# Kernel optimization log

Hardware: AMD Instinct MI355X
Metric: run time of the kernel (lower is better)

Reference implementation:

```python
import math
import jax, jax.numpy as jnp
import numpy as np


def _pairwise_sqdist(x, y):
    # x: [N, d], y: [M, d] -> [N, M]
    x2 = jnp.sum(x * x, axis=-1)[:, None]
    y2 = jnp.sum(y * y, axis=-1)[None, :]
    return jnp.maximum(x2 + y2 - 2.0 * (x @ y.T), 0.0)


def setup_inputs() -> dict:
    key = jax.random.key(0)
    k1, k2 = jax.random.split(key)
    N, M, D = 8192, 8192, 2
    base_points = jax.random.normal(k1, (N, D), dtype=jnp.float32)
    target_points = jax.random.normal(k2, (M, D), dtype=jnp.float32)
    log_sigma = jnp.asarray(math.log(0.1), dtype=jnp.float32)
    log_scale = jnp.zeros((D,), dtype=jnp.float32)
    return {
        "base_points": base_points,
        "target_points": target_points,
        "log_sigma": log_sigma,
        "log_scale": log_scale,
    }


def reference(base_points, target_points, log_sigma, log_scale):
    # learn_scale=True: anisotropic per-coordinate scaling
    scale = jnp.exp(log_scale)
    base = base_points * scale
    target = target_points * scale

    # uniform node weights (use_weight_net=False)
    N = base.shape[0]
    M = target.shape[0]
    w_base = jnp.full((N,), 1.0 / N, dtype=base.dtype)
    w_target = jnp.full((M,), 1.0 / M, dtype=target.dtype)

    # center=True: subtract weighted centroid of each cloud
    base = base - jnp.sum(w_base[:, None] * base, axis=0, keepdims=True)
    target = target - jnp.sum(w_target[:, None] * target, axis=0, keepdims=True)

    sigma = jnp.exp(log_sigma)
    inv2s2 = 1.0 / (2.0 * sigma * sigma)

    k_bb = jnp.exp(-_pairwise_sqdist(base, base) * inv2s2)      # [N, N]
    k_tt = jnp.exp(-_pairwise_sqdist(target, target) * inv2s2)  # [M, M]
    k_bt = jnp.exp(-_pairwise_sqdist(base, target) * inv2s2)    # [N, M]

    term_bb = w_base @ (k_bb @ w_base)
    term_tt = w_target @ (k_tt @ w_target)
    term_bt = w_base @ (k_bt @ w_target)
    loss = term_bb + term_tt - 2.0 * term_bt
    return loss
```

## Files before the change

### kernel.cpp

```cpp
#include <hip/hip_runtime.h>


#define BLOCK 256
#define NT_CROSS 512
#define NT_TOT   1056
#define LOG2E 1.4426950408889634f

typedef float v2f __attribute__((ext_vector_type(2)));

struct Prep { float f0, f1, sh0, sh1; };

__device__ __forceinline__ float fexp2(float x) {
    return __builtin_amdgcn_exp2f(x);
}

__global__ __launch_bounds__(1024) void prep_kernel(
    const float* __restrict__ base, const float* __restrict__ target,
    const float* __restrict__ log_sigma, const float* __restrict__ log_scale,
    int N, int M, Prep* __restrict__ pp, double* __restrict__ slots)
{
    __shared__ double mred[16][4];
    const int tid = threadIdx.x;
    if (tid < 64) slots[tid] = 0.0;

    double sbx = 0, sby = 0, stx = 0, sty = 0;
    const float4* b4 = (const float4*)base;
    const float4* t4 = (const float4*)target;
    for (int i = tid; i < (N >> 1); i += 1024) {
        float4 v = b4[i];
        sbx += (double)v.x + (double)v.z;
        sby += (double)v.y + (double)v.w;
    }
    for (int i = tid; i < (M >> 1); i += 1024) {
        float4 v = t4[i];
        stx += (double)v.x + (double)v.z;
        sty += (double)v.y + (double)v.w;
    }
    for (int off = 32; off; off >>= 1) {
        sbx += __shfl_down(sbx, off); sby += __shfl_down(sby, off);
        stx += __shfl_down(stx, off); sty += __shfl_down(sty, off);
    }
    if ((tid & 63) == 0) {
        mred[tid >> 6][0] = sbx; mred[tid >> 6][1] = sby;
        mred[tid >> 6][2] = stx; mred[tid >> 6][3] = sty;
    }
    __syncthreads();
    if (tid == 0) {
        double b0 = 0, b1 = 0, t0 = 0, t1 = 0;
        for (int k = 0; k < 16; ++k) {
            b0 += mred[k][0]; b1 += mred[k][1];
            t0 += mred[k][2]; t1 += mred[k][3];
        }
        float s0 = expf(log_scale[0]);
        float s1 = expf(log_scale[1]);
        float sigma = expf(log_sigma[0]);
        float inv2s2 = 1.0f / (2.0f * sigma * sigma);
        float sq = sqrtf(inv2s2 * LOG2E);
        float f0 = s0 * sq, f1 = s1 * sq;
        pp->f0 = f0; pp->f1 = f1;
        pp->sh0 = (float)(b0 / (double)N - t0 / (double)M) * f0;
        pp->sh1 = (float)(b1 / (double)N - t1 / (double)M) * f1;
    }
}

__global__ __launch_bounds__(BLOCK, 4) void mmd_main(
    const float* __restrict__ base, const float* __restrict__ target,
    int N, int M, const Prep* __restrict__ pp, double* __restrict__ slots)
{
    __shared__ __align__(16) float tbx[256];
    __shared__ __align__(16) float tby[256];
    __shared__ __align__(16) float tbc[256];
    __shared__ double wredd[4];

    const int tid = threadIdx.x;
    const int t   = blockIdx.x;
    const Prep p = *pp;
    const float2* base2   = (const float2*)base;
    const float2* target2 = (const float2*)target;

    const double wNN = 1.0 / ((double)N * (double)N);
    const double wMM = 1.0 / ((double)M * (double)M);
    const double wNM = -2.0 / ((double)N * (double)M);

    int ib, jb, term;
    bool diag;
    const float2* A2;
    const float2* B2;
    double wt;
    float shx = 0.f, shy = 0.f;
    if (t < NT_CROSS) {
        ib = t >> 5; jb = t & 31;
        A2 = base2; B2 = target2;
        wt = wNM; diag = false; term = 2;
        shx = p.sh0; shy = p.sh1;
    } else {
        const int u = t - NT_CROSS;
        term = (u >= 272) ? 1 : 0;
        const int v = u - term * 272;
        int r = (int)((33.0f - sqrtf(1089.0f - 4.0f * (float)v)) * 0.5f);
        r = min(max(r, 0), 15);
        while (r > 0 && r * (33 - r) > v) --r;
        while (r < 15 && (r + 1) * (32 - r) <= v) ++r;
        ib = r;
        jb = 2 * r + (v - r * (33 - r));
        diag = (jb <= 2 * r + 1);
        A2 = term ? target2 : base2;  B2 = A2;
        wt = 2.0 * (term ? wMM : wNN);
    }
    const int i0 = ib * 512, j0 = jb * 256;

    {
        float2 b = B2[j0 + tid];
        float bx = b.x * p.f0, by = b.y * p.f1;
        tbx[tid] = bx;
        tby[tid] = by;
        tbc[tid] = -fmaf(bx, bx, by * by);
    }
    __syncthreads();

    const int r0  = i0 + (tid & 127);
    const int js  = (tid >> 7) * 128;

    float ax2s[4], ay2s[4], A0s[4];
#pragma unroll
    for (int k = 0; k < 4; ++k) {
        float2 a = A2[r0 + 128 * k];
        float ax = fmaf(a.x, p.f0, -shx);
        float ay = fmaf(a.y, p.f1, -shy);
        ax2s[k] = ax + ax;
        ay2s[k] = ay + ay;
        A0s[k]  = -fmaf(ax, ax, ay * ay);
    }

    const float4* bx4 = (const float4*)(tbx + js);
    const float4* by4 = (const float4*)(tby + js);
    const float4* c4  = (const float4*)(tbc + js);

    double result;
    if (!diag) {
        v2f s[4][2];
#pragma unroll
        for (int k = 0; k < 4; ++k) { s[k][0] = (v2f){0.f, 0.f}; s[k][1] = (v2f){0.f, 0.f}; }
#pragma unroll 4
        for (int q = 0; q < 32; ++q) {
            float4 BX = bx4[q];
            float4 BY = by4[q];
            float4 C  = c4[q];
            v2f bx01 = { BX.x, BX.y }, bx23 = { BX.z, BX.w };
            v2f by01 = { BY.x, BY.y }, by23 = { BY.z, BY.w };
            v2f c01  = { C.x,  C.y  }, c23  = { C.z,  C.w  };
#pragma unroll
            for (int k = 0; k < 4; ++k) {
                v2f A0v  = { A0s[k],  A0s[k]  };
                v2f ax2v = { ax2s[k], ax2s[k] };
                v2f ay2v = { ay2s[k], ay2s[k] };
                v2f e01 = ax2v * bx01 + (ay2v * by01 + (c01 + A0v));
                v2f e23 = ax2v * bx23 + (ay2v * by23 + (c23 + A0v));
                s[k][0] += (v2f){ fexp2(e01.x), fexp2(e01.y) };
                s[k][1] += (v2f){ fexp2(e23.x), fexp2(e23.y) };
            }
        }
        double tot = 0.0;
#pragma unroll
        for (int k = 0; k < 4; ++k) {
            v2f st = s[k][0] + s[k][1];
            tot += (double)(st.x + st.y);
        }
        result = wt * tot;
    } else {
        float sge = 0.f, sgt = 0.f;
        const int jbase = j0 + js;
#pragma unroll 2
        for (int q = 0; q < 32; ++q) {
            float4 BX = bx4[q];
            float4 BY = by4[q];
            float4 C  = c4[q];
            const int j = jbase + 4 * q;
#pragma unroll
            for (int k = 0; k < 4; ++k) {
                const int row = r0 + 128 * k;
                float e0 = fmaf(ax2s[k], BX.x, fmaf(ay2s[k], BY.x, C.x + A0s[k]));
                float e1 = fmaf(ax2s[k], BX.y, fmaf(ay2s[k], BY.y, C.y + A0s[k]));
                float e2 = fmaf(ax2s[k], BX.z, fmaf(ay2s[k], BY.z, C.z + A0s[k]));
                float e3 = fmaf(ax2s[k], BX.w, fmaf(ay2s[k], BY.w, C.w + A0s[k]));
                float v0 = fexp2(e0), v1 = fexp2(e1);
                float v2 = fexp2(e2), v3 = fexp2(e3);
                sge += (j + 0 >= row) ? v0 : 0.f;  sgt += (j + 0 > row) ? v0 : 0.f;
                sge += (j + 1 >= row) ? v1 : 0.f;  sgt += (j + 1 > row) ? v1 : 0.f;
                sge += (j + 2 >= row) ? v2 : 0.f;  sgt += (j + 2 > row) ? v2 : 0.f;
                sge += (j + 3 >= row) ? v3 : 0.f;  sgt += (j + 3 > row) ? v3 : 0.f;
            }
        }
        result = (term ? wMM : wNN) * (double)(sge + sgt);
    }

    for (int off = 32; off; off >>= 1) result += __shfl_down(result, off);
    if ((tid & 63) == 0) wredd[tid >> 6] = result;
    __syncthreads();
    if (tid == 0) {
        double s = wredd[0] + wredd[1] + wredd[2] + wredd[3];
        atomicAdd(&slots[t & 63], s);
    }
}

__global__ void final_kernel(const double* __restrict__ slots,
                             float* __restrict__ out)
{
    const int tid = threadIdx.x;
    double s = slots[tid];
    for (int off = 32; off; off >>= 1) s += __shfl_down(s, off);
    if (tid == 0) out[0] = (float)s;
}

extern "C" void kernel_launch(void* const* d_in, const int* in_sizes, int n_in,
                              void* d_out, int out_size, void* d_ws, size_t ws_size,
                              hipStream_t stream)
{
    const float* base      = (const float*)d_in[0];
    const float* target    = (const float*)d_in[1];
    const float* log_sigma = (const float*)d_in[2];
    const float* log_scale = (const float*)d_in[3];
    float* out = (float*)d_out;

    int N = in_sizes[0] / 2;
    int M = in_sizes[1] / 2;

    Prep*   pp    = (Prep*)d_ws;
    double* slots = (double*)((char*)d_ws + 64);

    prep_kernel<<<1, 1024, 0, stream>>>(base, target, log_sigma, log_scale,
                                        N, M, pp, slots);
    mmd_main<<<NT_TOT, BLOCK, 0, stream>>>(base, target, N, M, pp, slots);
    final_kernel<<<1, 64, 0, stream>>>(slots, out);
}
```

Measured before the change: 100.3 us.

## Shrink tiles to 256x256 and double grid for finer-grained work distribution

Tile height drops from 512 to 256 rows, so each thread handles 2 rows instead of 4. The cross grid doubles to 1024 blocks and the triangular self-term mapping is recomputed for a 32x32 tile grid, giving 2080 blocks in total. Launch bounds now ask for 8 blocks per CU. The aim is better load balance and occupancy across CUs, at the cost of less reuse per LDS load, more block overhead, and more diagonal tiles that take the slower masked path.

Result: faster. 90.53 us (-9.7%).

```diff
diff --git a/kernel.cpp b/kernel.cpp
--- a/kernel.cpp
+++ b/kernel.cpp
@@ -2,8 +2,8 @@
 
 
 #define BLOCK 256
-#define NT_CROSS 512
-#define NT_TOT   1056
+#define NT_CROSS 1024
+#define NT_TOT   2080
 #define LOG2E 1.4426950408889634f
 
 typedef float v2f __attribute__((ext_vector_type(2)));
@@ -63,7 +63,7 @@
     }
 }
 
-__global__ __launch_bounds__(BLOCK, 4) void mmd_main(
+__global__ __launch_bounds__(BLOCK, 8) void mmd_main(
     const float* __restrict__ base, const float* __restrict__ target,
     int N, int M, const Prep* __restrict__ pp, double* __restrict__ slots)
 {
@@ -95,19 +95,19 @@
         shx = p.sh0; shy = p.sh1;
     } else {
         const int u = t - NT_CROSS;
-        term = (u >= 272) ? 1 : 0;
-        const int v = u - term * 272;
-        int r = (int)((33.0f - sqrtf(1089.0f - 4.0f * (float)v)) * 0.5f);
-        r = min(max(r, 0), 15);
-        while (r > 0 && r * (33 - r) > v) --r;
-        while (r < 15 && (r + 1) * (32 - r) <= v) ++r;
+        term = (u >= 528) ? 1 : 0;
+        const int v = u - term * 528;
+        int r = (int)((65.0f - sqrtf(4225.0f - 8.0f * (float)v)) * 0.5f);
+        r = min(max(r, 0), 31);
+        while (r > 0 && (r * (65 - r)) / 2 > v) --r;
+        while (r < 31 && ((r + 1) * (64 - r)) / 2 <= v) ++r;
         ib = r;
-        jb = 2 * r + (v - r * (33 - r));
-        diag = (jb <= 2 * r + 1);
+        jb = r + (v - (r * (65 - r)) / 2);
+        diag = (jb == ib);
         A2 = term ? target2 : base2;  B2 = A2;
         wt = 2.0 * (term ? wMM : wNN);
     }
-    const int i0 = ib * 512, j0 = jb * 256;
+    const int i0 = ib * 256, j0 = jb * 256;
 
     {
         float2 b = B2[j0 + tid];
@@ -118,12 +118,12 @@
     }
     __syncthreads();
 
-    const int r0  = i0 + (tid & 127);
-    const int js  = (tid >> 7) * 128;
-
-    float ax2s[4], ay2s[4], A0s[4];
+    const int r0 = i0 + (tid & 127);
+    const int js = (tid >> 7) * 128;
+
+    float ax2s[2], ay2s[2], A0s[2];
 #pragma unroll
-    for (int k = 0; k < 4; ++k) {
+    for (int k = 0; k < 2; ++k) {
         float2 a = A2[r0 + 128 * k];
         float ax = fmaf(a.x, p.f0, -shx);
         float ay = fmaf(a.y, p.f1, -shy);
@@ -138,35 +138,38 @@
 
     double result;
     if (!diag) {
-        v2f s[4][2];
-#pragma unroll
-        for (int k = 0; k < 4; ++k) { s[k][0] = (v2f){0.f, 0.f}; s[k][1] = (v2f){0.f, 0.f}; }
+        v2f s00 = {0.f, 0.f}, s01 = {0.f, 0.f};
+        v2f s10 = {0.f, 0.f}, s11 = {0.f, 0.f};
 #pragma unroll 4
         for (int q = 0; q < 32; ++q) {
             float4 BX = bx4[q];
             float4 BY = by4[q];
             float4 C  = c4[q];
-            v2f bx01 = { BX.x, BX.y }, bx23 = { BX.z, BX.w };
-            v2f by01 = { BY.x, BY.y }, by23 = { BY.z, BY.w };
-            v2f c01  = { C.x,  C.y  }, c23  = { C.z,  C.w  };
-#pragma unroll
-            for (int k = 0; k < 4; ++k) {
-                v2f A0v  = { A0s[k],  A0s[k]  };
-                v2f ax2v = { ax2s[k], ax2s[k] };
-                v2f ay2v = { ay2s[k], ay2s[k] };
-                v2f e01 = ax2v * bx01 + (ay2v * by01 + (c01 + A0v));
-                v2f e23 = ax2v * bx23 + (ay2v * by23 + (c23 + A0v));
-                s[k][0] += (v2f){ fexp2(e01.x), fexp2(e01.y) };
-                s[k][1] += (v2f){ fexp2(e23.x), fexp2(e23.y) };
+            v2f bxa = { BX.x, BX.y }, bxb = { BX.z, BX.w };
+            v2f bya = { BY.x, BY.y }, byb = { BY.z, BY.w };
+            v2f ca  = { C.x,  C.y  }, cb  = { C.z,  C.w  };
+            {
+                v2f A0v = { A0s[0], A0s[0] };
+                v2f axv = { ax2s[0], ax2s[0] };
+                v2f ayv = { ay2s[0], ay2s[0] };
+                v2f ea = axv * bxa + (ayv * bya + (ca + A0v));
+                v2f eb = axv * bxb + (ayv * byb + (cb + A0v));
+                s00 += (v2f){ fexp2(ea.x), fexp2(ea.y) };
+                s01 += (v2f){ fexp2(eb.x), fexp2(eb.y) };
+            }
+            {
+                v2f A0v = { A0s[1], A0s[1] };
+                v2f axv = { ax2s[1], ax2s[1] };
+                v2f ayv = { ay2s[1], ay2s[1] };
+                v2f ea = axv * bxa + (ayv * bya + (ca + A0v));
+                v2f eb = axv * bxb + (ayv * byb + (cb + A0v));
+                s10 += (v2f){ fexp2(ea.x), fexp2(ea.y) };
+                s11 += (v2f){ fexp2(eb.x), fexp2(eb.y) };
             }
         }
-        double tot = 0.0;
-#pragma unroll
-        for (int k = 0; k < 4; ++k) {
-            v2f st = s[k][0] + s[k][1];
-            tot += (double)(st.x + st.y);
-        }
-        result = wt * tot;
+        v2f st0 = s00 + s01;
+        v2f st1 = s10 + s11;
+        result = wt * ((double)(st0.x + st0.y) + (double)(st1.x + st1.y));
     } else {
         float sge = 0.f, sgt = 0.f;
         const int jbase = j0 + js;
@@ -177,7 +180,7 @@
             float4 C  = c4[q];
             const int j = jbase + 4 * q;
 #pragma unroll
-            for (int k = 0; k < 4; ++k) {
+            for (int k = 0; k < 2; ++k) {
                 const int row = r0 + 128 * k;
                 float e0 = fmaf(ax2s[k], BX.x, fmaf(ay2s[k], BY.x, C.x + A0s[k]));
                 float e1 = fmaf(ax2s[k], BX.y, fmaf(ay2s[k], BY.y, C.y + A0s[k]));
```
